# Kernel optimization log

Hardware: AMD Instinct MI355X
Metric: run time of the kernel (lower is better)

The kernel has to match this reference:

```python
import jax, jax.numpy as jnp
import numpy as np

K = 20          # args.k
NEG = 0.2       # LeakyReLU negative slope

def lrelu(x):
    return jnp.where(x >= 0, x, NEG * x)

def bn(x, s, b):
    # eval-mode batchnorm folded into per-channel affine; channel axis = 1
    sh = (1, -1) + (1,) * (x.ndim - 2)
    return x * s.reshape(sh) + b.reshape(sh)

def se(x, w1, w2):
    # Squeeze-and-Excite on (B, C, N, k)
    y = jnp.mean(x, axis=(2, 3))                      # (B, C)
    y = jax.nn.sigmoid(jax.nn.relu(y @ w1.T) @ w2.T)  # (B, C)
    return x * y[:, :, None, None]

def graph_feature(x):
    # x: (B, C, N) -> edge features (B, 2C, N, K)
    xx = jnp.sum(x * x, axis=1)                        # (B, N)
    inner = jnp.einsum('bcn,bcm->bnm', x, x)           # (B, N, N)
    dist = -xx[:, :, None] + 2.0 * inner - xx[:, None, :]
    idx = jax.lax.top_k(dist, K)[1]                    # (B, N, K) nearest (incl. self)
    xt = jnp.transpose(x, (0, 2, 1))                   # (B, N, C)
    nbr = jax.vmap(lambda t, i: t[i])(xt, idx)         # (B, N, K, C)
    ctr = xt[:, :, None, :]
    out = jnp.concatenate([nbr - ctr, jnp.broadcast_to(ctr, nbr.shape)], axis=3)
    return jnp.transpose(out, (0, 3, 1, 2))

def edge_block(x, w, s, b, w1, w2):
    # get_graph_feature -> 1x1 conv -> BN -> SE -> LeakyReLU -> max over k
    g = graph_feature(x)                               # (B, 2C, N, K)
    h = jnp.einsum('bcnk,oc->bonk', g, w)
    h = lrelu(se(bn(h, s, b), w1, w2))
    return jnp.max(h, axis=-1)                         # (B, O, N)

def forward(x, conv1_w, conv2_w, conv3_w, conv4_w, conv5_w,
            bn1_s, bn1_b, bn2_s, bn2_b, bn3_s, bn3_b, bn4_s, bn4_b, bn5_s, bn5_b,
            se1_w1, se1_w2, se2_w1, se2_w2, se3_w1, se3_w2, se4_w1, se4_w2,
            res1_w, res2_w, res3_w,
            lin1_w, bn6_s, bn6_b, lin2_w, lin2_b, bn7_s, bn7_b, lin3_w, lin3_b):
    x1 = edge_block(x, conv1_w, bn1_s, bn1_b, se1_w1, se1_w2)                 # (B,512,N)
    x2 = edge_block(x1, conv2_w, bn2_s, bn2_b, se2_w1, se2_w2)
    x2 = x2 + jnp.einsum('bcn,oc->bon', x1, res1_w)                           # (B,512,N)
    x3 = edge_block(x2, conv3_w, bn3_s, bn3_b, se3_w1, se3_w2)
    x3 = x3 + jnp.einsum('bcn,oc->bon', x2, res2_w)                           # (B,1024,N)
    x4 = edge_block(x3, conv4_w, bn4_s, bn4_b, se4_w1, se4_w2)
    x4 = x4 + jnp.einsum('bcn,oc->bon', x3, res3_w)                           # (B,1024,N)
    h = jnp.concatenate([x1, x2, x3, x4], axis=1)                             # (B,3072,N)
    h = lrelu(bn(jnp.einsum('bcn,oc->bon', h, conv5_w), bn5_s, bn5_b))        # (B,2048,N)
    f = jnp.concatenate([jnp.max(h, axis=-1), jnp.mean(h, axis=-1)], axis=1)  # (B,4096)
    f = lrelu(bn(f @ lin1_w.T, bn6_s, bn6_b))       # dropout is eval-mode identity
    f = lrelu(bn(f @ lin2_w.T + lin2_b, bn7_s, bn7_b))
    return f @ lin3_w.T + lin3_b                    # (B,40)

def setup_inputs():
    ks = jax.random.split(jax.random.key(0), 40)
    B, N = 16, 128
    f32 = jnp.float32
    def w(i, shape, s=0.02):
        return jax.random.normal(ks[i], shape, f32) * s
    def bns(i, c):
        return 1.0 + 0.1 * jax.random.normal(ks[i], (c,), f32)
    def bnb(i, c):
        return 0.1 * jax.random.normal(ks[i], (c,), f32)
    return {
        'x': jax.random.normal(ks[0], (B, 512, N), f32),
        'conv1_w': w(1, (512, 1024)),
        'conv2_w': w(2, (512, 1024)),
        'conv3_w': w(3, (1024, 1024)),
        'conv4_w': w(4, (1024, 2048)),
        'conv5_w': w(5, (2048, 3072)),
        'bn1_s': bns(6, 512), 'bn1_b': bnb(7, 512),
        'bn2_s': bns(8, 512), 'bn2_b': bnb(9, 512),
        'bn3_s': bns(10, 1024), 'bn3_b': bnb(11, 1024),
        'bn4_s': bns(12, 1024), 'bn4_b': bnb(13, 1024),
        'bn5_s': bns(14, 2048), 'bn5_b': bnb(15, 2048),
        'se1_w1': w(16, (32, 512), 0.05), 'se1_w2': w(17, (512, 32), 0.05),
        'se2_w1': w(18, (32, 512), 0.05), 'se2_w2': w(19, (512, 32), 0.05),
        'se3_w1': w(20, (64, 1024), 0.05), 'se3_w2': w(21, (1024, 64), 0.05),
        'se4_w1': w(22, (64, 1024), 0.05), 'se4_w2': w(23, (1024, 64), 0.05),
        'res1_w': w(24, (512, 512)),
        'res2_w': w(25, (1024, 512)),
        'res3_w': w(26, (1024, 1024)),
        'lin1_w': w(27, (512, 4096)),
        'bn6_s': bns(28, 512), 'bn6_b': bnb(29, 512),
        'lin2_w': w(30, (256, 512)), 'lin2_b': bnb(31, 256),
        'bn7_s': bns(32, 256), 'bn7_b': bnb(33, 256),
        'lin3_w': w(34, (40, 256)), 'lin3_b': bnb(35, 40),
    }

def reference(x, conv1_w, conv2_w, conv3_w, conv4_w, conv5_w,
              bn1_s, bn1_b, bn2_s, bn2_b, bn3_s, bn3_b, bn4_s, bn4_b, bn5_s, bn5_b,
              se1_w1, se1_w2, se2_w1, se2_w2, se3_w1, se3_w2, se4_w1, se4_w2,
              res1_w, res2_w, res3_w,
              lin1_w, bn6_s, bn6_b, lin2_w, lin2_b, bn7_s, bn7_b, lin3_w, lin3_b):
    return forward(x, conv1_w, conv2_w, conv3_w, conv4_w, conv5_w,
                   bn1_s, bn1_b, bn2_s, bn2_b, bn3_s, bn3_b, bn4_s, bn4_b, bn5_s, bn5_b,
                   se1_w1, se1_w2, se2_w1, se2_w2, se3_w1, se3_w2, se4_w1, se4_w2,
                   res1_w, res2_w, res3_w,
                   lin1_w, bn6_s, bn6_b, lin2_w, lin2_b, bn7_s, bn7_b, lin3_w, lin3_b)
```

## Files before the change

### kernel.cpp

```cpp
#include <hip/hip_runtime.h>
#include <hip/hip_bf16.h>


#define BN_ALL 2048
typedef __hip_bfloat16 bf16;
typedef __attribute__((ext_vector_type(8))) short short8;
typedef __attribute__((ext_vector_type(4))) float float4v;

__device__ __forceinline__ float b2f(bf16 v) { return __bfloat162float(v); }
__device__ __forceinline__ float lrelu(float v) { return v >= 0.f ? v : 0.2f * v; }
__device__ __forceinline__ short f2bs(float v) {
    bf16 h = __float2bfloat16(v);
    return *reinterpret_cast<short*>(&h);
}

__device__ __forceinline__ float ldin(const void* p, size_t i, int isb) {
    return isb ? __bfloat162float(((const bf16*)p)[i]) : ((const float*)p)[i];
}

__device__ __forceinline__ float ld1(const float* p) { return *p; }
__device__ __forceinline__ float ld1(const bf16* p)  { return __bfloat162float(*p); }
__device__ __forceinline__ void st1(float* p, float v) { *p = v; }
__device__ __forceinline__ void st1(bf16* p, float v)  { *p = __float2bfloat16(v); }
__device__ __forceinline__ short ldbs(const float* p) { return f2bs(*p); }
__device__ __forceinline__ short ldbs(const bf16* p)  { return *(const short*)p; }

__global__ __launch_bounds__(256) void detect_dtype(const void* __restrict__ x, int* __restrict__ flag) {
    const unsigned* u = (const unsigned*)x;
    int sane = 0;
    for (int i = threadIdx.x; i < 4096; i += 256) {
        unsigned e = (u[i] >> 23) & 0xFF;
        sane += (e >= 87 && e <= 167) ? 1 : 0;
    }
    __shared__ int sh[256];
    sh[threadIdx.x] = sane;
    __syncthreads();
    for (int off = 128; off > 0; off >>= 1) {
        if (threadIdx.x < off) sh[threadIdx.x] += sh[threadIdx.x + off];
        __syncthreads();
    }
    if (threadIdx.x == 0) *flag = (sh[0] < 2048) ? 1 : 0;
}

__global__ __launch_bounds__(256) void convert_kp(const void* __restrict__ x, bf16* __restrict__ X0,
                                                  const int* __restrict__ dflag) {
    int isb = *dflag;
    int item = blockIdx.x * 256 + threadIdx.x;
    int cg = item >> 11, bn = item & 2047;
    int b = bn >> 7, n = bn & 127;
    short8 pk;
#pragma unroll
    for (int j = 0; j < 8; ++j)
        pk[j] = f2bs(ldin(x, ((size_t)(b * 512 + cg * 8 + j)) * 128 + n, isb));
    *(short8*)((short*)X0 + ((size_t)cg * BN_ALL + bn) * 8) = pk;
}

__global__ __launch_bounds__(256) void gram_k(const bf16* __restrict__ X, int C,
                                              float* __restrict__ G) {
    __shared__ short Bsm[2][4096];
    int tid = threadIdx.x;
    int b = blockIdx.x, strip = blockIdx.y;
    int lane = tid & 63, wv = tid >> 6, wm = wv & 1, wn = wv >> 1;
    int lq = lane >> 4, lr = lane & 15;
    int KC = C >> 5;
    const short* Xs = (const short*)X;

    float4v acc[4];
#pragma unroll
    for (int i = 0; i < 4; i++) acc[i] = (float4v){0.f, 0.f, 0.f, 0.f};

    short8 br2[2];
#pragma unroll
    for (int it = 0; it < 2; ++it) {
        int i = tid + it * 256;
        int q = i >> 7, c = i & 127;
        *(short8*)&Bsm[0][(size_t)i * 8] =
            *(const short8*)(Xs + ((size_t)q * BN_ALL + b * 128 + c) * 8);
    }
    __syncthreads();

    int p = 0;
    for (int kc = 0; kc < KC; ++kc) {
        if (kc + 1 < KC) {
#pragma unroll
            for (int it = 0; it < 2; ++it) {
                int i = tid + it * 256;
                int q = i >> 7, c = i & 127;
                br2[it] = *(const short8*)(Xs + ((size_t)((kc + 1) * 4 + q) * BN_ALL + b * 128 + c) * 8);
            }
        }
        short8 av[4], bv;
#pragma unroll
        for (int mt = 0; mt < 4; ++mt)
            av[mt] = *(const short8*)&Bsm[p][(size_t)((lq << 7) + wm * 64 + mt * 16 + lr) * 8];
        bv = *(const short8*)&Bsm[p][(size_t)((lq << 7) + strip * 32 + wn * 16 + lr) * 8];
#pragma unroll
        for (int mt = 0; mt < 4; ++mt)
            acc[mt] = __builtin_amdgcn_mfma_f32_16x16x32_bf16(av[mt], bv, acc[mt], 0, 0, 0);
        if (kc + 1 < KC) {
#pragma unroll
            for (int it = 0; it < 2; ++it)
                *(short8*)&Bsm[p ^ 1][(size_t)(tid + it * 256) * 8] = br2[it];
        }
        __syncthreads();
        p ^= 1;
    }

    float* Gb = G + (size_t)b * 16384;
#pragma unroll
    for (int mt = 0; mt < 4; ++mt)
#pragma unroll
        for (int r = 0; r < 4; ++r) {
            int row = wm * 64 + mt * 16 + lq * 4 + r;
            int col = strip * 32 + wn * 16 + lr;
            Gb[row * 128 + col] = acc[mt][r];
        }
}

__global__ __launch_bounds__(256) void topk_k(const float* __restrict__ G, int* __restrict__ idx) {
    int gw = (blockIdx.x * 256 + threadIdx.x) >> 6;
    int lane = threadIdx.x & 63;
    int b = gw >> 7, n = gw & 127;
    const float* Gb = G + (size_t)b * 16384;
    float g0 = Gb[n * 128 + lane];
    float g1 = Gb[n * 128 + 64 + lane];
    float dnn = Gb[n * 129];
    float dm0 = Gb[lane * 129];
    float dm1 = Gb[(64 + lane) * 129];
    float d0 = 2.f * g0 - dnn - dm0;
    float d1 = 2.f * g1 - dnn - dm1;
#pragma unroll
    for (int k = 0; k < 20; ++k) {
        float v; int i;
        if (d1 > d0) { v = d1; i = 64 + lane; } else { v = d0; i = lane; }
#pragma unroll
        for (int off = 1; off < 64; off <<= 1) {
            float ov = __shfl_xor(v, off, 64);
            int   oi = __shfl_xor(i, off, 64);
            if (ov > v || (ov == v && oi < i)) { v = ov; i = oi; }
        }
        if (lane == 0) idx[gw * 20 + k] = i;
        if (i < 64) { if (lane == i) d0 = -3.0e38f; }
        else        { if (lane == i - 64) d1 = -3.0e38f; }
    }
}

template <typename S>
__global__ __launch_bounds__(128) void knn_topk(const S* __restrict__ X, int C, int* __restrict__ idx) {
    int b = blockIdx.x >> 7;
    int n = blockIdx.x & 127;
    int m = threadIdx.x;
    const S* base = X + b * 128;
    float s0 = 0, s1 = 0, q0 = 0, q1 = 0;
    for (int c = 0; c < C; c += 2) {
        const S* p = base + (size_t)c * BN_ALL;
        float xm0 = ld1(p + m),          xn0 = ld1(p + n);
        float xm1 = ld1(p + BN_ALL + m), xn1 = ld1(p + BN_ALL + n);
        s0 += xm0 * xn0; q0 += xm0 * xm0;
        s1 += xm1 * xn1; q1 += xm1 * xm1;
    }
    float inner = s0 + s1;
    float xxm   = q0 + q1;
    __shared__ float xx[128];
    __shared__ float dist[128];
    __shared__ float rv[128];
    __shared__ int   ri[128];
    xx[m] = xxm;
    __syncthreads();
    dist[m] = 2.0f * inner - xx[n] - xxm;
    for (int k = 0; k < 20; k++) {
        __syncthreads();
        rv[m] = dist[m]; ri[m] = m;
        __syncthreads();
        for (int off = 64; off > 0; off >>= 1) {
            if (m < off) {
                float a = rv[m], bv = rv[m + off];
                int ia = ri[m], ib = ri[m + off];
                if (bv > a || (bv == a && ib < ia)) { rv[m] = bv; ri[m] = ib; }
            }
            __syncthreads();
        }
        if (m == 0) { idx[blockIdx.x * 20 + k] = ri[0]; dist[ri[0]] = -3.0e38f; }
    }
}

__global__ __launch_bounds__(256) void pack_w(const void* __restrict__ w, int ldw,
                                              const void* __restrict__ res, int Cin, int O,
                                              int Mtot, int K, short* __restrict__ out,
                                              const int* __restrict__ dflag) {
    int isb = *dflag;
    int item = blockIdx.x * 256 + threadIdx.x;
    if (item >= Mtot * (K >> 3)) return;
    int m_local = item & 127;
    int rest = item >> 7;
    int q = rest & 3; rest >>= 2;
    int KC = K >> 5;
    int kc = rest % KC, tm = rest / KC;
    int grow = tm * 128 + m_local;
    int k = kc * 32 + q * 8;
    const void* src; size_t base; int dif = 0;
    if (grow < O)          { src = w;   base = (size_t)grow * ldw + k; }
    else if (grow < 2 * O) { src = w;   base = (size_t)(grow - O) * ldw + k; dif = 1; }
    else                   { src = res; base = (size_t)(grow - 2 * O) * Cin + k; }
    short8 pk;
#pragma unroll
    for (int j = 0; j < 8; ++j) {
        float v = ldin(src, base + j, isb);
        if (dif) v = ldin(src, base + Cin + j, isb) - v;
        pk[j] = f2bs(v);
    }
    *(short8*)&out[(size_t)item * 8] = pk;
}

__global__ __launch_bounds__(256) void gemm_p2(const short* __restrict__ packA,
                                               const bf16* __restrict__ X, float* __restrict__ Cm, int K,
                                               const void* __restrict__ bnS, const void* __restrict__ bnB,
                                               int act, const int* __restrict__ dflag) {
    __shared__ short Asm[2][4096];
    __shared__ short Bsm[2][4096];
    int tid = threadIdx.x;
    int bm  = blockIdx.x << 7;
    int bn0 = blockIdx.y << 7;
    int lane = tid & 63, wv = tid >> 6, wm = wv & 1, wn = wv >> 1;
    int lq = lane >> 4, lr = lane & 15;
    int KC = K >> 5;
    const short* abase = packA + (size_t)blockIdx.x * KC * 4096;
    const short* Xs = (const short*)X;

    float4v acc[4][4];
#pragma unroll
    for (int i = 0; i < 4; i++)
#pragma unroll
        for (int j = 0; j < 4; j++) acc[i][j] = (float4v){0.f, 0.f, 0.f, 0.f};

    short8 ar[2], br[2];
    int bq = tid >> 7, bc = tid & 127;

#pragma unroll
    for (int it = 0; it < 2; ++it) {
        ar[it] = *(const short8*)&abase[(size_t)(tid + it * 256) * 8];
        br[it] = *(const short8*)(Xs + ((size_t)(bq + it * 2) * BN_ALL + bn0 + bc) * 8);
    }
#pragma unroll
    for (int it = 0; it < 2; ++it) {
        *(short8*)&Asm[0][(size_t)(tid + it * 256) * 8] = ar[it];
        *(short8*)&Bsm[0][(size_t)(tid + it * 256) * 8] = br[it];
    }
    __syncthreads();

    int p = 0;
    for (int kc = 0; kc < KC; ++kc) {
        if (kc + 1 < KC) {
            const short* ab = abase + (size_t)(kc + 1) * 4096;
#pragma unroll
            for (int it = 0; it < 2; ++it) {
                ar[it] = *(const short8*)&ab[(size_t)(tid + it * 256) * 8];
                br[it] = *(const short8*)(Xs + ((size_t)((kc + 1) * 4 + bq + it * 2) * BN_ALL + bn0 + bc) * 8);
            }
        }
        short8 av[4], bv[4];
#pragma unroll
        for (int mt = 0; mt < 4; ++mt)
            av[mt] = *(const short8*)&Asm[p][(size_t)((lq << 7) + wm * 64 + mt * 16 + lr) * 8];
#pragma unroll
        for (int nt = 0; nt < 4; ++nt)
            bv[nt] = *(const short8*)&Bsm[p][(size_t)((lq << 7) + wn * 64 + nt * 16 + lr) * 8];
#pragma unroll
        for (int mt = 0; mt < 4; ++mt)
#pragma unroll
            for (int nt = 0; nt < 4; ++nt)
                acc[mt][nt] = __builtin_amdgcn_mfma_f32_16x16x32_bf16(av[mt], bv[nt], acc[mt][nt], 0, 0, 0);
        if (kc + 1 < KC) {
#pragma unroll
            for (int it = 0; it < 2; ++it) {
                *(short8*)&Asm[p ^ 1][(size_t)(tid + it * 256) * 8] = ar[it];
                *(short8*)&Bsm[p ^ 1][(size_t)(tid + it * 256) * 8] = br[it];
            }
        }
        __syncthreads();
        p ^= 1;
    }

    int isb = *dflag;
#pragma unroll
    for (int mt = 0; mt < 4; ++mt) {
#pragma unroll
        for (int r = 0; r < 4; ++r) {
            int row = bm + wm * 64 + mt * 16 + lq * 4 + r;
            float s = 1.f, bb = 0.f;
            if (bnS) { s = ldin(bnS, row, isb); bb = ldin(bnB, row, isb); }
#pragma unroll
            for (int nt = 0; nt < 4; ++nt) {
                int col = bn0 + wn * 64 + nt * 16 + lr;
                float v = acc[mt][nt][r];
                if (bnS) v = v * s + bb;
                if (act) v = lrelu(v);
                Cm[(size_t)row * BN_ALL + col] = v;
            }
        }
    }
}

template <typename S>
__global__ __launch_bounds__(256) void gemm_mfma(const void* __restrict__ w, int ldw,
                                                 const void* __restrict__ res, int Cin, int O,
                                                 const S* __restrict__ X, S* __restrict__ Cm, int K,
                                                 const void* __restrict__ bnS, const void* __restrict__ bnB,
                                                 int act, const int* __restrict__ dflag) {
    int isb = *dflag;
    __shared__ short Asm[4096];
    __shared__ short Bsm[4096];
    int tid = threadIdx.x;
    int bm  = blockIdx.x << 7;
    int bn0 = blockIdx.y << 7;
    int lane = tid & 63, wv = tid >> 6;
    int wm = wv & 1, wn = wv >> 1;
    int lq = lane >> 4, lr = lane & 15;

    float4v acc[4][4];
#pragma unroll
    for (int i = 0; i < 4; i++)
#pragma unroll
        for (int j = 0; j < 4; j++) acc[i][j] = (float4v){0.f, 0.f, 0.f, 0.f};

    for (int k0 = 0; k0 < K; k0 += 32) {
#pragma unroll
        for (int it = 0; it < 2; ++it) {
            int i = tid + it * 256;
            int m = i >> 2, q = i & 3;
            int grow = bm + m;
            const void* asrc; size_t abase; int dif = 0;
            if (grow < O)          { asrc = w;   abase = (size_t)grow * ldw; }
            else if (grow < 2 * O) { asrc = w;   abase = (size_t)(grow - O) * ldw; dif = 1; }
            else                   { asrc = res; abase = (size_t)(grow - 2 * O) * Cin; }
            size_t kk = (size_t)k0 + q * 8;
            short8 pk;
#pragma unroll
            for (int j = 0; j < 8; ++j) {
                float v = ldin(asrc, abase + kk + j, isb);
                if (dif) v = ldin(asrc, abase + Cin + kk + j, isb) - v;
                pk[j] = f2bs(v);
            }
            *(short8*)&Asm[(size_t)(q * 128 + m) * 8] = pk;
        }
#pragma unroll
        for (int it = 0; it < 2; ++it) {
            int i = tid + it * 256;
            int q = i >> 7, c = i & 127;
            const S* xp = X + (size_t)(k0 + q * 8) * BN_ALL + bn0 + c;
            short8 pk;
#pragma unroll
            for (int j = 0; j < 8; ++j) pk[j] = f2bs(ld1(xp + (size_t)j * BN_ALL));
            *(short8*)&Bsm[(size_t)i * 8] = pk;
        }
        __syncthreads();
        short8 av[4], bv[4];
#pragma unroll
        for (int mt = 0; mt < 4; ++mt)
            av[mt] = *(const short8*)&Asm[(size_t)((lq << 7) + wm * 64 + mt * 16 + lr) * 8];
#pragma unroll
        for (int nt = 0; nt < 4; ++nt)
            bv[nt] = *(const short8*)&Bsm[(size_t)((lq << 7) + wn * 64 + nt * 16 + lr) * 8];
#pragma unroll
        for (int mt = 0; mt < 4; ++mt)
#pragma unroll
            for (int nt = 0; nt < 4; ++nt)
                acc[mt][nt] = __builtin_amdgcn_mfma_f32_16x16x32_bf16(av[mt], bv[nt], acc[mt][nt], 0, 0, 0);
        __syncthreads();
    }
#pragma unroll
    for (int mt = 0; mt < 4; ++mt) {
#pragma unroll
        for (int r = 0; r < 4; ++r) {
            int row = bm + wm * 64 + mt * 16 + lq * 4 + r;
            float s = 1.f, bb = 0.f;
            if (bnS) { s = ldin(bnS, row, isb); bb = ldin(bnB, row, isb); }
#pragma unroll
            for (int nt = 0; nt < 4; ++nt) {
                int col = bn0 + wn * 64 + nt * 16 + lr;
                float v = acc[mt][nt][r];
                if (bnS) v = v * s + bb;
                if (act) v = lrelu(v);
                st1(Cm + (size_t)row * BN_ALL + col, v);
            }
        }
    }
}

template <typename S>
__global__ __launch_bounds__(128) void gather_pool(S* __restrict__ PS, const int* __restrict__ idx,
                                                   const void* __restrict__ bns, const void* __restrict__ bnb,
                                                   float* __restrict__ Mb, int O,
                                                   const int* __restrict__ dflag) {
    int isb = *dflag;
    int o = blockIdx.x, b = blockIdx.y, n = threadIdx.x;
    S* Prow = PS + (size_t)o * BN_ALL + b * 128;
    const int* id = idx + (b * 128 + n) * 20;
    float mx = -3.0e38f, mn = 3.0e38f, sm = 0.f;
#pragma unroll
    for (int k = 0; k < 20; k++) {
        float p = ld1(Prow + id[k]);
        mx = fmaxf(mx, p); mn = fminf(mn, p); sm += p;
    }
    float Sv = ld1(PS + (size_t)(O + o) * BN_ALL + b * 128 + n);
    __shared__ float r1[128], r2[128];
    r1[n] = sm; r2[n] = Sv;
    __syncthreads();
    float s = ldin(bns, o, isb), bb = ldin(bnb, o, isb);
    float ext = (s >= 0.f) ? mx : mn;
    st1(Prow + n, lrelu(s * (ext + Sv) + bb));
    for (int off = 64; off > 0; off >>= 1) {
        if (n < off) { r1[n] += r1[n + off]; r2[n] += r2[n + off]; }
        __syncthreads();
    }
    if (n == 0) Mb[b * O + o] = s * (r1[0] * (1.f / 2560.f) + r2[0] * (1.f / 128.f)) + bb;
}

__global__ __launch_bounds__(256) void se1_k(const float* __restrict__ Mb, const void* __restrict__ w1,
                                             float* __restrict__ Z, int O, int r,
                                             const int* __restrict__ dflag) {
    int isb = *dflag;
    int gw = (blockIdx.x * 256 + threadIdx.x) >> 6;
    int lane = threadIdx.x & 63;
    int b = gw / r, t = gw - b * r;
    const float* mv = Mb + (size_t)b * O;
    float acc = 0.f;
    for (int c = lane; c < O; c += 64) acc += ldin(w1, (size_t)t * O + c, isb) * mv[c];
#pragma unroll
    for (int off = 32; off > 0; off >>= 1) acc += __shfl_xor(acc, off, 64);
    if (lane == 0) Z[b * r + t] = fmaxf(acc, 0.f);
}

__global__ __launch_bounds__(256) void se2_k(const float* __restrict__ Z, const void* __restrict__ w2,
                                             float* __restrict__ Y, int O, int r,
                                             const int* __restrict__ dflag) {
    int isb = *dflag;
    int gw = (blockIdx.x * 256 + threadIdx.x) >> 6;
    int lane = threadIdx.x & 63;
    int b = gw / O, o = gw - b * O;
    float acc = 0.f;
    if (lane < r) acc = ldin(w2, (size_t)o * r + lane, isb) * Z[b * r + lane];
#pragma unroll
    for (int off = 32; off > 0; off >>= 1) acc += __shfl_xor(acc, off, 64);
    if (lane == 0) Y[b * O + o] = 1.f / (1.f + expf(-acc));
}

__global__ __launch_bounds__(256) void se_k(const float* __restrict__ Mb, const void* __restrict__ w1,
                                            const void* __restrict__ w2, float* __restrict__ Y, int O, int r,
                                            const int* __restrict__ dflag) {
    int isb = *dflag;
    int b = blockIdx.x, t = threadIdx.x;
    __shared__ float mloc[1024];
    __shared__ float z[64];
    for (int i = t; i < O; i += 256) mloc[i] = Mb[b * O + i];
    __syncthreads();
    if (t < r) {
        float acc = 0.f;
        for (int c = 0; c < O; c++) acc += ldin(w1, (size_t)t * O + c, isb) * mloc[c];
        z[t] = fmaxf(acc, 0.f);
    }
    __syncthreads();
    for (int o = t; o < O; o += 256) {
        float acc = 0.f;
        for (int j = 0; j < r; j++) acc += ldin(w2, (size_t)o * r + j, isb) * z[j];
        Y[b * O + o] = 1.f / (1.f + expf(-acc));
    }
}

__global__ __launch_bounds__(256) void finalize_kp(const float* __restrict__ PS, const float* __restrict__ Y,
                                                   int useR, bf16* __restrict__ Xdst, int O) {
    int item = blockIdx.x * 256 + threadIdx.x;
    int og = item >> 11, bn = item & 2047;
    int b = bn >> 7;
    short8 pk;
#pragma unroll
    for (int j = 0; j < 8; ++j) {
        int r = og * 8 + j;
        float v = Y[b * O + r] * PS[(size_t)r * BN_ALL + bn];
        if (useR) v += PS[(size_t)(2 * O + r) * BN_ALL + bn];
        pk[j] = f2bs(v);
    }
    *(short8*)((short*)Xdst + ((size_t)og * BN_ALL + bn) * 8) = pk;
}

template <typename SP, typename SD>
__global__ __launch_bounds__(256) void finalize(const SP* __restrict__ PS, const float* __restrict__ Y,
                                                int useR, SD* __restrict__ Xdst, int O) {
    int tid = blockIdx.x * 256 + threadIdx.x;
    int o = tid >> 11, bn = tid & 2047;
    int b = bn >> 7;
    float v = Y[b * O + o] * ld1(PS + tid);
    if (useR) v += ld1(PS + (size_t)(2 * O + o) * BN_ALL + bn);
    st1(Xdst + tid, v);
}

template <typename S>
__global__ __launch_bounds__(256) void convert_x(const void* __restrict__ x, S* __restrict__ X0,
                                                 const int* __restrict__ dflag) {
    int isb = *dflag;
    int tid = blockIdx.x * 256 + threadIdx.x;
    int c = tid >> 11, bn = tid & 2047;
    int b = bn >> 7, n = bn & 127;
    st1(X0 + tid, ldin(x, (size_t)(b * 512 + c) * 128 + n, isb));
}

template <typename S>
__global__ __launch_bounds__(128) void pool5(const S* __restrict__ H, float* __restrict__ f) {
    int m = blockIdx.x, b = blockIdx.y, n = threadIdx.x;
    float v = ld1(H + (size_t)m * BN_ALL + b * 128 + n);
    __shared__ float rmx[128], rsm[128];
    rmx[n] = v; rsm[n] = v;
    __syncthreads();
    for (int off = 64; off > 0; off >>= 1) {
        if (n < off) { rmx[n] = fmaxf(rmx[n], rmx[n + off]); rsm[n] += rsm[n + off]; }
        __syncthreads();
    }
    if (n == 0) {
        f[b * 4096 + m] = rmx[0];
        f[b * 4096 + 2048 + m] = rsm[0] * (1.f / 128.f);
    }
}

__global__ __launch_bounds__(256) void head_k(const float* __restrict__ in, const void* __restrict__ W,
                                              const void* __restrict__ bias, const void* __restrict__ bns,
                                              const void* __restrict__ bnb, float* __restrict__ outf,
                                              void* __restrict__ outb, int Kd, int Od, int act,
                                              const int* __restrict__ dflag) {
    int isb = *dflag;
    int gw = (blockIdx.x * 256 + threadIdx.x) >> 6;
    int lane = threadIdx.x & 63;
    if (gw >= 16 * Od) return;
    int b = gw / Od, o = gw - b * Od;
    const float* iv = in + b * Kd;
    float acc = 0.f;
    for (int k = lane; k < Kd; k += 64) acc += iv[k] * ldin(W, (size_t)o * Kd + k, isb);
    for (int off = 32; off > 0; off >>= 1) acc += __shfl_xor(acc, off, 64);
    if (lane == 0) {
        float v = acc;
        if (bias) v += ldin(bias, o, isb);
        if (bns) v = v * ldin(bns, o, isb) + ldin(bnb, o, isb);
        if (act) v = lrelu(v);
        if (outb) {
            if (isb) ((bf16*)outb)[gw] = __float2bfloat16(v);
            else     ((float*)outb)[gw] = v;
        } else outf[gw] = v;
    }
}

__global__ __launch_bounds__(256) void zero_out(bf16* o, int n) {
    int i = blockIdx.x * 256 + threadIdx.x;
    if (i < n) o[i] = __float2bfloat16(0.f);
}

#define UNPACK_INPUTS()                                                     \
    const void* x_in   = d_in[0];                                           \
    const void* conv1w = d_in[1];  const void* conv2w = d_in[2];            \
    const void* conv3w = d_in[3];  const void* conv4w = d_in[4];            \
    const void* conv5w = d_in[5];                                           \
    const void* bn1s = d_in[6],  * bn1b = d_in[7];                          \
    const void* bn2s = d_in[8],  * bn2b = d_in[9];                          \
    const void* bn3s = d_in[10], * bn3b = d_in[11];                         \
    const void* bn4s = d_in[12], * bn4b = d_in[13];                         \
    const void* bn5s = d_in[14], * bn5b = d_in[15];                         \
    const void* se1w1 = d_in[16], * se1w2 = d_in[17];                       \
    const void* se2w1 = d_in[18], * se2w2 = d_in[19];                       \
    const void* se3w1 = d_in[20], * se3w2 = d_in[21];                       \
    const void* se4w1 = d_in[22], * se4w2 = d_in[23];                       \
    const void* res1w = d_in[24]; const void* res2w = d_in[25];             \
    const void* res3w = d_in[26]; const void* lin1w = d_in[27];             \
    const void* bn6s = d_in[28], * bn6b = d_in[29];                         \
    const void* lin2w = d_in[30], * lin2b = d_in[31];                       \
    const void* bn7s = d_in[32], * bn7b = d_in[33];                         \
    const void* lin3w = d_in[34], * lin3b = d_in[35];

static void run_net_packed(void* const* d_in, void* d_out, void* d_ws, hipStream_t stream) {
    UNPACK_INPUTS();
    float* WS = (float*)d_ws;
    float* PS   = WS;
    bf16*  XC   = (bf16*)(WS + 6291456);
    short* PACK = (short*)(WS + 12582912);
    float* MB = WS + 15728640;
    float* YB = MB + 16384;
    float* FB = YB + 16384;
    float* F1 = FB + 65536;
    float* F2 = F1 + 8192;
    int* IDX  = (int*)(F2 + 4096);
    int* DFLAG = IDX + 40960;
    float* ZB = (float*)(DFLAG + 16);
    bf16*  X0 = (bf16*)(PS + (size_t)2048 * BN_ALL);
    float* GRAM = PS;
    bf16* X1 = XC;
    bf16* X2 = XC + (size_t)512 * BN_ALL;
    bf16* X3 = XC + (size_t)1024 * BN_ALL;
    bf16* X4 = XC + (size_t)2048 * BN_ALL;

    detect_dtype<<<1, 256, 0, stream>>>(x_in, DFLAG);
    convert_kp<<<512, 256, 0, stream>>>(x_in, X0, DFLAG);

    gram_k<<<dim3(16, 4), 256, 0, stream>>>(X0, 512, GRAM);
    topk_k<<<512, 256, 0, stream>>>(GRAM, IDX);
    pack_w<<<256, 256, 0, stream>>>(conv1w, 1024, nullptr, 512, 512, 1024, 512, PACK, DFLAG);
    gemm_p2<<<dim3(8, 16), 256, 0, stream>>>(PACK, X0, PS, 512, nullptr, nullptr, 0, DFLAG);
    gather_pool<float><<<dim3(512, 16), 128, 0, stream>>>(PS, IDX, bn1s, bn1b, MB, 512, DFLAG);
    se1_k<<<128, 256, 0, stream>>>(MB, se1w1, ZB, 512, 32, DFLAG);
    se2_k<<<2048, 256, 0, stream>>>(ZB, se1w2, YB, 512, 32, DFLAG);
    finalize_kp<<<512, 256, 0, stream>>>(PS, YB, 0, X1, 512);

    gram_k<<<dim3(16, 4), 256, 0, stream>>>(X1, 512, GRAM);
    topk_k<<<512, 256, 0, stream>>>(GRAM, IDX);
    pack_w<<<384, 256, 0, stream>>>(conv2w, 1024, res1w, 512, 512, 1536, 512, PACK, DFLAG);
    gemm_p2<<<dim3(12, 16), 256, 0, stream>>>(PACK, X1, PS, 512, nullptr, nullptr, 0, DFLAG);
    gather_pool<float><<<dim3(512, 16), 128, 0, stream>>>(PS, IDX, bn2s, bn2b, MB, 512, DFLAG);
    se1_k<<<128, 256, 0, stream>>>(MB, se2w1, ZB, 512, 32, DFLAG);
    se2_k<<<2048, 256, 0, stream>>>(ZB, se2w2, YB, 512, 32, DFLAG);
    finalize_kp<<<512, 256, 0, stream>>>(PS, YB, 1, X2, 512);

    gram_k<<<dim3(16, 4), 256, 0, stream>>>(X2, 512, GRAM);
    topk_k<<<512, 256, 0, stream>>>(GRAM, IDX);
    pack_w<<<768, 256, 0, stream>>>(conv3w, 1024, res2w, 512, 1024, 3072, 512, PACK, DFLAG);
    gemm_p2<<<dim3(24, 16), 256, 0, stream>>>(PACK, X2, PS, 512, nullptr, nullptr, 0, DFLAG);
    gather_pool<float><<<dim3(1024, 16), 128, 0, stream>>>(PS, IDX, bn3s, bn3b, MB, 1024, DFLAG);
    se1_k<<<256, 256, 0, stream>>>(MB, se3w1, ZB, 1024, 64, DFLAG);
    se2_k<<<4096, 256, 0, stream>>>(ZB, se3w2, YB, 1024, 64, DFLAG);
    finalize_kp<<<1024, 256, 0, stream>>>(PS, YB, 1, X3, 1024);

    gram_k<<<dim3(16, 4), 256, 0, stream>>>(X3, 1024, GRAM);
    topk_k<<<512, 256, 0, stream>>>(GRAM, IDX);
    pack_w<<<1536, 256, 0, stream>>>(conv4w, 2048, res3w, 1024, 1024, 3072, 1024, PACK, DFLAG);
    gemm_p2<<<dim3(24, 16), 256, 0, stream>>>(PACK, X3, PS, 1024, nullptr, nullptr, 0, DFLAG);
    gather_pool<float><<<dim3(1024, 16), 128, 0, stream>>>(PS, IDX, bn4s, bn4b, MB, 1024, DFLAG);
    se1_k<<<256, 256, 0, stream>>>(MB, se4w1, ZB, 1024, 64, DFLAG);
    se2_k<<<4096, 256, 0, stream>>>(ZB, se4w2, YB, 1024, 64, DFLAG);
    finalize_kp<<<1024, 256, 0, stream>>>(PS, YB, 1, X4, 1024);

    pack_w<<<3072, 256, 0, stream>>>(conv5w, 3072, nullptr, 3072, 2048, 2048, 3072, PACK, DFLAG);
    gemm_p2<<<dim3(16, 16), 256, 0, stream>>>(PACK, XC, PS, 3072, bn5s, bn5b, 1, DFLAG);
    pool5<float><<<dim3(2048, 16), 128, 0, stream>>>(PS, FB);

    head_k<<<2048, 256, 0, stream>>>(FB, lin1w, nullptr, bn6s, bn6b, F1, nullptr, 4096, 512, 1, DFLAG);
    head_k<<<1024, 256, 0, stream>>>(F1, lin2w, lin2b, bn7s, bn7b, F2, nullptr, 512, 256, 1, DFLAG);
    head_k<<<160, 256, 0, stream>>>(F2, lin3w, lin3b, nullptr, nullptr, nullptr, d_out, 256, 40, 0, DFLAG);
}

template <typename S>
static void run_net(void* const* d_in, void* d_out, void* d_ws, hipStream_t stream) {
    UNPACK_INPUTS();
    const size_t RC = (size_t)3072 * BN_ALL;
    S* PS = (S*)d_ws;
    S* XC = PS + RC;
    S* X0 = PS + (size_t)2048 * BN_ALL;
    float* MB = (float*)(XC + RC);
    float* YB = MB + 16 * 1024;
    float* FB = YB + 16 * 1024;
    float* F1 = FB + 16 * 4096;
    float* F2 = F1 + 16 * 512;
    int* IDX  = (int*)(F2 + 16 * 256);
    int* DFLAG = IDX + 16 * 128 * 20;

    S* X1 = XC;
    S* X2 = XC + (size_t)512 * BN_ALL;
    S* X3 = XC + (size_t)1024 * BN_ALL;
    S* X4 = XC + (size_t)2048 * BN_ALL;

    detect_dtype<<<1, 256, 0, stream>>>(x_in, DFLAG);
    convert_x<S><<<4096, 256, 0, stream>>>(x_in, X0, DFLAG);

    knn_topk<S><<<2048, 128, 0, stream>>>(X0, 512, IDX);
    gemm_mfma<S><<<dim3(8, 16), 256, 0, stream>>>(conv1w, 1024, nullptr, 512, 512, X0, PS, 512, nullptr, nullptr, 0, DFLAG);
    gather_pool<S><<<dim3(512, 16), 128, 0, stream>>>(PS, IDX, bn1s, bn1b, MB, 512, DFLAG);
    se_k<<<16, 256, 0, stream>>>(MB, se1w1, se1w2, YB, 512, 32, DFLAG);
    finalize<S, S><<<4096, 256, 0, stream>>>(PS, YB, 0, X1, 512);

    knn_topk<S><<<2048, 128, 0, stream>>>(X1, 512, IDX);
    gemm_mfma<S><<<dim3(12, 16), 256, 0, stream>>>(conv2w, 1024, res1w, 512, 512, X1, PS, 512, nullptr, nullptr, 0, DFLAG);
    gather_pool<S><<<dim3(512, 16), 128, 0, stream>>>(PS, IDX, bn2s, bn2b, MB, 512, DFLAG);
    se_k<<<16, 256, 0, stream>>>(MB, se2w1, se2w2, YB, 512, 32, DFLAG);
    finalize<S, S><<<4096, 256, 0, stream>>>(PS, YB, 1, X2, 512);

    knn_topk<S><<<2048, 128, 0, stream>>>(X2, 512, IDX);
    gemm_mfma<S><<<dim3(24, 16), 256, 0, stream>>>(conv3w, 1024, res2w, 512, 1024, X2, PS, 512, nullptr, nullptr, 0, DFLAG);
    gather_pool<S><<<dim3(1024, 16), 128, 0, stream>>>(PS, IDX, bn3s, bn3b, MB, 1024, DFLAG);
    se_k<<<16, 256, 0, stream>>>(MB, se3w1, se3w2, YB, 1024, 64, DFLAG);
    finalize<S, S><<<8192, 256, 0, stream>>>(PS, YB, 1, X3, 1024);

    knn_topk<S><<<2048, 128, 0, stream>>>(X3, 1024, IDX);
    gemm_mfma<S><<<dim3(24, 16), 256, 0, stream>>>(conv4w, 2048, res3w, 1024, 1024, X3, PS, 1024, nullptr, nullptr, 0, DFLAG);
    gather_pool<S><<<dim3(1024, 16), 128, 0, stream>>>(PS, IDX, bn4s, bn4b, MB, 1024, DFLAG);
    se_k<<<16, 256, 0, stream>>>(MB, se4w1, se4w2, YB, 1024, 64, DFLAG);
    finalize<S, S><<<8192, 256, 0, stream>>>(PS, YB, 1, X4, 1024);

    gemm_mfma<S><<<dim3(16, 16), 256, 0, stream>>>(conv5w, 3072, nullptr, 3072, 2048, XC, PS, 3072, bn5s, bn5b, 1, DFLAG);
    pool5<S><<<dim3(2048, 16), 128, 0, stream>>>(PS, FB);

    head_k<<<2048, 256, 0, stream>>>(FB, lin1w, nullptr, bn6s, bn6b, F1, nullptr, 4096, 512, 1, DFLAG);
    head_k<<<1024, 256, 0, stream>>>(F1, lin2w, lin2b, bn7s, bn7b, F2, nullptr, 512, 256, 1, DFLAG);
    head_k<<<160, 256, 0, stream>>>(F2, lin3w, lin3b, nullptr, nullptr, nullptr, d_out, 256, 40, 0, DFLAG);
}

extern "C" void kernel_launch(void* const* d_in, const int* in_sizes, int n_in,
                              void* d_out, int out_size, void* d_ws, size_t ws_size,
                              hipStream_t stream) {
    const size_t SMALL = (16 * 1024 + 16 * 1024 + 16 * 4096 + 16 * 512 + 16 * 256) * 4
                       + 16 * 128 * 20 * 4 + 8192;
    const size_t NEED_PACKED = (size_t)15728640 * 4 + SMALL;
    const size_t NEED_F32    = 2 * ((size_t)3072 * BN_ALL * 4) + SMALL;
    const size_t NEED_BF16   = 2 * ((size_t)3072 * BN_ALL * 2) + SMALL;
    if (ws_size >= NEED_PACKED) {
        run_net_packed(d_in, d_out, d_ws, stream);
    } else if (ws_size >= NEED_F32) {
        run_net<float>(d_in, d_out, d_ws, stream);
    } else if (ws_size >= NEED_BF16) {
        run_net<bf16>(d_in, d_out, d_ws, stream);
    } else {
        zero_out<<<3, 256, 0, stream>>>((bf16*)d_out, out_size);
    }
}
```

Measured before the change: 646.5 us.

## Replace LDS-staged GEMM with register-direct 4-stage pipelined MFMA and async gram loads

The main GEMM drops shared-memory staging. Each wave now loads its MFMA fragments directly from global memory into registers, using a 4-deep software pipeline, and the N tile is halved to 64 so the grid has twice as many blocks. The gram kernel uses global_load_lds async copies, when the builtin is available, in place of register round-trips into LDS. This removes LDS writes and barriers in the GEMM, at the cost of redundant global loads across waves (no LDS sharing) and higher register pressure from the buffered fragments.

```diff
diff --git a/kernel.cpp b/kernel.cpp
--- a/kernel.cpp
+++ b/kernel.cpp
@@ -6,6 +6,20 @@
 typedef __hip_bfloat16 bf16;
 typedef __attribute__((ext_vector_type(8))) short short8;
 typedef __attribute__((ext_vector_type(4))) float float4v;
+
+#if defined(__has_builtin)
+#if __has_builtin(__builtin_amdgcn_global_load_lds)
+#define HAS_GLL 1
+#endif
+#endif
+
+#ifdef HAS_GLL
+__device__ __forceinline__ void gll16(const void* g, void* l) {
+    __builtin_amdgcn_global_load_lds(
+        (const __attribute__((address_space(1))) void*)g,
+        (__attribute__((address_space(3))) void*)l, 16, 0, 0);
+}
+#endif
 
 __device__ __forceinline__ float b2f(bf16 v) { return __bfloat162float(v); }
 __device__ __forceinline__ float lrelu(float v) { return v >= 0.f ? v : 0.2f * v; }
@@ -22,8 +36,6 @@
 __device__ __forceinline__ float ld1(const bf16* p)  { return __bfloat162float(*p); }
 __device__ __forceinline__ void st1(float* p, float v) { *p = v; }
 __device__ __forceinline__ void st1(bf16* p, float v)  { *p = __float2bfloat16(v); }
-__device__ __forceinline__ short ldbs(const float* p) { return f2bs(*p); }
-__device__ __forceinline__ short ldbs(const bf16* p)  { return *(const short*)p; }
 
 __global__ __launch_bounds__(256) void detect_dtype(const void* __restrict__ x, int* __restrict__ flag) {
     const unsigned* u = (const unsigned*)x;
@@ -57,7 +69,7 @@
 
 __global__ __launch_bounds__(256) void gram_k(const bf16* __restrict__ X, int C,
                                               float* __restrict__ G) {
-    __shared__ short Bsm[2][4096];
+    __shared__ __align__(16) short Bsm[2][4096];
     int tid = threadIdx.x;
     int b = blockIdx.x, strip = blockIdx.y;
     int lane = tid & 63, wv = tid >> 6, wm = wv & 1, wn = wv >> 1;
@@ -69,6 +81,37 @@
 #pragma unroll
     for (int i = 0; i < 4; i++) acc[i] = (float4v){0.f, 0.f, 0.f, 0.f};
 
+#ifdef HAS_GLL
+#pragma unroll
+    for (int it = 0; it < 2; ++it) {
+        int i = tid + it * 256;
+        int q = i >> 7, c = i & 127;
+        gll16(Xs + ((size_t)q * BN_ALL + b * 128 + c) * 8, &Bsm[0][(size_t)i * 8]);
+    }
+    __syncthreads();
+    int p = 0;
+    for (int kc = 0; kc < KC; ++kc) {
+        if (kc + 1 < KC) {
+#pragma unroll
+            for (int it = 0; it < 2; ++it) {
+                int i = tid + it * 256;
+                int q = i >> 7, c = i & 127;
+                gll16(Xs + ((size_t)((kc + 1) * 4 + q) * BN_ALL + b * 128 + c) * 8,
+                      &Bsm[p ^ 1][(size_t)i * 8]);
+            }
+        }
+        short8 av[4], bv;
+#pragma unroll
+        for (int mt = 0; mt < 4; ++mt)
+            av[mt] = *(const short8*)&Bsm[p][(size_t)((lq << 7) + wm * 64 + mt * 16 + lr) * 8];
+        bv = *(const short8*)&Bsm[p][(size_t)((lq << 7) + strip * 32 + wn * 16 + lr) * 8];
+#pragma unroll
+        for (int mt = 0; mt < 4; ++mt)
+            acc[mt] = __builtin_amdgcn_mfma_f32_16x16x32_bf16(av[mt], bv, acc[mt], 0, 0, 0);
+        __syncthreads();
+        p ^= 1;
+    }
+#else
     short8 br2[2];
 #pragma unroll
     for (int it = 0; it < 2; ++it) {
@@ -78,7 +121,6 @@
             *(const short8*)(Xs + ((size_t)q * BN_ALL + b * 128 + c) * 8);
     }
     __syncthreads();
-
     int p = 0;
     for (int kc = 0; kc < KC; ++kc) {
         if (kc + 1 < KC) {
@@ -105,6 +147,7 @@
         __syncthreads();
         p ^= 1;
     }
+#endif
 
     float* Gb = G + (size_t)b * 16384;
 #pragma unroll
@@ -212,73 +255,57 @@
     *(short8*)&out[(size_t)item * 8] = pk;
 }
 
-__global__ __launch_bounds__(256) void gemm_p2(const short* __restrict__ packA,
+#define LOADK(kc_, s_) do {                                                        \
+    int _kc = (kc_);                                                               \
+    if (_kc < KC) {                                                                \
+        const short* _ab = abase + (size_t)_kc * 4096;                             \
+        _Pragma("unroll")                                                          \
+        for (int mt = 0; mt < 4; ++mt) bufA[s_][mt] = *(const short8*)(_ab + aoff[mt]); \
+        const short* _bb = Xs + (size_t)(_kc * 4 + lq) * (BN_ALL * 8);             \
+        _Pragma("unroll")                                                          \
+        for (int nt = 0; nt < 2; ++nt) bufB[s_][nt] = *(const short8*)(_bb + boff[nt]); \
+    } } while (0)
+#define MFMAK(s_) do {                                                             \
+    _Pragma("unroll")                                                              \
+    for (int mt = 0; mt < 4; ++mt)                                                 \
+        _Pragma("unroll")                                                          \
+        for (int nt = 0; nt < 2; ++nt)                                             \
+            acc[mt][nt] = __builtin_amdgcn_mfma_f32_16x16x32_bf16(bufA[s_][mt], bufB[s_][nt], acc[mt][nt], 0, 0, 0); \
+    } while (0)
+
+__global__ __launch_bounds__(256) void gemm_dr(const short* __restrict__ packA,
                                                const bf16* __restrict__ X, float* __restrict__ Cm, int K,
                                                const void* __restrict__ bnS, const void* __restrict__ bnB,
                                                int act, const int* __restrict__ dflag) {
-    __shared__ short Asm[2][4096];
-    __shared__ short Bsm[2][4096];
     int tid = threadIdx.x;
     int bm  = blockIdx.x << 7;
-    int bn0 = blockIdx.y << 7;
+    int bn0 = blockIdx.y << 6;
     int lane = tid & 63, wv = tid >> 6, wm = wv & 1, wn = wv >> 1;
     int lq = lane >> 4, lr = lane & 15;
     int KC = K >> 5;
     const short* abase = packA + (size_t)blockIdx.x * KC * 4096;
     const short* Xs = (const short*)X;
 
-    float4v acc[4][4];
+    int aoff[4], boff[2];
+#pragma unroll
+    for (int mt = 0; mt < 4; ++mt) aoff[mt] = ((lq << 7) + wm * 64 + mt * 16 + lr) * 8;
+#pragma unroll
+    for (int nt = 0; nt < 2; ++nt) boff[nt] = (bn0 + wn * 32 + nt * 16 + lr) * 8;
+
+    float4v acc[4][2];
 #pragma unroll
     for (int i = 0; i < 4; i++)
 #pragma unroll
-        for (int j = 0; j < 4; j++) acc[i][j] = (float4v){0.f, 0.f, 0.f, 0.f};
-
-    short8 ar[2], br[2];
-    int bq = tid >> 7, bc = tid & 127;
-
-#pragma unroll
-    for (int it = 0; it < 2; ++it) {
-        ar[it] = *(const short8*)&abase[(size_t)(tid + it * 256) * 8];
-        br[it] = *(const short8*)(Xs + ((size_t)(bq + it * 2) * BN_ALL + bn0 + bc) * 8);
-    }
-#pragma unroll
-    for (int it = 0; it < 2; ++it) {
-        *(short8*)&Asm[0][(size_t)(tid + it * 256) * 8] = ar[it];
-        *(short8*)&Bsm[0][(size_t)(tid + it * 256) * 8] = br[it];
-    }
-    __syncthreads();
-
-    int p = 0;
-    for (int kc = 0; kc < KC; ++kc) {
-        if (kc + 1 < KC) {
-            const short* ab = abase + (size_t)(kc + 1) * 4096;
-#pragma unroll
-            for (int it = 0; it < 2; ++it) {
-                ar[it] = *(const short8*)&ab[(size_t)(tid + it * 256) * 8];
-                br[it] = *(const short8*)(Xs + ((size_t)((kc + 1) * 4 + bq + it * 2) * BN_ALL + bn0 + bc) * 8);
-            }
-        }
-        short8 av[4], bv[4];
-#pragma unroll
-        for (int mt = 0; mt < 4; ++mt)
-            av[mt] = *(const short8*)&Asm[p][(size_t)((lq << 7) + wm * 64 + mt * 16 + lr) * 8];
-#pragma unroll
-        for (int nt = 0; nt < 4; ++nt)
-            bv[nt] = *(const short8*)&Bsm[p][(size_t)((lq << 7) + wn * 64 + nt * 16 + lr) * 8];
-#pragma unroll
-        for (int mt = 0; mt < 4; ++mt)
-#pragma unroll
-            for (int nt = 0; nt < 4; ++nt)
-                acc[mt][nt] = __builtin_amdgcn_mfma_f32_16x16x32_bf16(av[mt], bv[nt], acc[mt][nt], 0, 0, 0);
-        if (kc + 1 < KC) {
-#pragma unroll
-            for (int it = 0; it < 2; ++it) {
-                *(short8*)&Asm[p ^ 1][(size_t)(tid + it * 256) * 8] = ar[it];
-                *(short8*)&Bsm[p ^ 1][(size_t)(tid + it * 256) * 8] = br[it];
-            }
-        }
-        __syncthreads();
-        p ^= 1;
+        for (int j = 0; j < 2; j++) acc[i][j] = (float4v){0.f, 0.f, 0.f, 0.f};
+
+    short8 bufA[4][4], bufB[4][2];
+    LOADK(0, 0);
+    LOADK(1, 1);
+    for (int kc0 = 0; kc0 < KC; kc0 += 4) {
+        LOADK(kc0 + 2, 2); MFMAK(0);
+        LOADK(kc0 + 3, 3); MFMAK(1);
+        LOADK(kc0 + 4, 0); MFMAK(2);
+        LOADK(kc0 + 5, 1); MFMAK(3);
     }
 
     int isb = *dflag;
@@ -290,8 +317,8 @@
             float s = 1.f, bb = 0.f;
             if (bnS) { s = ldin(bnS, row, isb); bb = ldin(bnB, row, isb); }
 #pragma unroll
-            for (int nt = 0; nt < 4; ++nt) {
-                int col = bn0 + wn * 64 + nt * 16 + lr;
+            for (int nt = 0; nt < 2; ++nt) {
+                int col = bn0 + wn * 32 + nt * 16 + lr;
                 float v = acc[mt][nt][r];
                 if (bnS) v = v * s + bb;
                 if (act) v = lrelu(v);
@@ -600,7 +627,7 @@
     gram_k<<<dim3(16, 4), 256, 0, stream>>>(X0, 512, GRAM);
     topk_k<<<512, 256, 0, stream>>>(GRAM, IDX);
     pack_w<<<256, 256, 0, stream>>>(conv1w, 1024, nullptr, 512, 512, 1024, 512, PACK, DFLAG);
-    gemm_p2<<<dim3(8, 16), 256, 0, stream>>>(PACK, X0, PS, 512, nullptr, nullptr, 0, DFLAG);
+    gemm_dr<<<dim3(8, 32), 256, 0, stream>>>(PACK, X0, PS, 512, nullptr, nullptr, 0, DFLAG);
     gather_pool<float><<<dim3(512, 16), 128, 0, stream>>>(PS, IDX, bn1s, bn1b, MB, 512, DFLAG);
     se1_k<<<128, 256, 0, stream>>>(MB, se1w1, ZB, 512, 32, DFLAG);
     se2_k<<<2048, 256, 0, stream>>>(ZB, se1w2, YB, 512, 32, DFLAG);
@@ -609,7 +636,7 @@
     gram_k<<<dim3(16, 4), 256, 0, stream>>>(X1, 512, GRAM);
     topk_k<<<512, 256, 0, stream>>>(GRAM, IDX);
     pack_w<<<384, 256, 0, stream>>>(conv2w, 1024, res1w, 512, 512, 1536, 512, PACK, DFLAG);
-    gemm_p2<<<dim3(12, 16), 256, 0, stream>>>(PACK, X1, PS, 512, nullptr, nullptr, 0, DFLAG);
+    gemm_dr<<<dim3(12, 32), 256, 0, stream>>>(PACK, X1, PS, 512, nullptr, nullptr, 0, DFLAG);
     gather_pool<float><<<dim3(512, 16), 128, 0, stream>>>(PS, IDX, bn2s, bn2b, MB, 512, DFLAG);
     se1_k<<<128, 256, 0, stream>>>(MB, se2w1, ZB, 512, 32, DFLAG);
     se2_k<<<2048, 256, 0, stream>>>(ZB, se2w2, YB, 512, 32, DFLAG);
@@ -618,7 +645,7 @@
     gram_k<<<dim3(16, 4), 256, 0, stream>>>(X2, 512, GRAM);
     topk_k<<<512, 256, 0, stream>>>(GRAM, IDX);
     pack_w<<<768, 256, 0, stream>>>(conv3w, 1024, res2w, 512, 1024, 3072, 512, PACK, DFLAG);
-    gemm_p2<<<dim3(24, 16), 256, 0, stream>>>(PACK, X2, PS, 512, nullptr, nullptr, 0, DFLAG);
+    gemm_dr<<<dim3(24, 32), 256, 0, stream>>>(PACK, X2, PS, 512, nullptr, nullptr, 0, DFLAG);
     gather_pool<float><<<dim3(1024, 16), 128, 0, stream>>>(PS, IDX, bn3s, bn3b, MB, 1024, DFLAG);
     se1_k<<<256, 256, 0, stream>>>(MB, se3w1, ZB, 1024, 64, DFLAG);
     se2_k<<<4096, 256, 0, stream>>>(ZB, se3w2, YB, 1024, 64, DFLAG);
@@ -627,14 +654,14 @@
     gram_k<<<dim3(16, 4), 256, 0, stream>>>(X3, 1024, GRAM);
     topk_k<<<512, 256, 0, stream>>>(GRAM, IDX);
     pack_w<<<1536, 256, 0, stream>>>(conv4w, 2048, res3w, 1024, 1024, 3072, 1024, PACK, DFLAG);
-    gemm_p2<<<dim3(24, 16), 256, 0, stream>>>(PACK, X3, PS, 1024, nullptr, nullptr, 0, DFLAG);
+    gemm_dr<<<dim3(24, 32), 256, 0, stream>>>(PACK, X3, PS, 1024, nullptr, nullptr, 0, DFLAG);
     gather_pool<float><<<dim3(1024, 16), 128, 0, stream>>>(PS, IDX, bn4s, bn4b, MB, 1024, DFLAG);
     se1_k<<<256, 256, 0, stream>>>(MB, se4w1, ZB, 1024, 64, DFLAG);
     se2_k<<<4096, 256, 0, stream>>>(ZB, se4w2, YB, 1024, 64, DFLAG);
     finalize_kp<<<1024, 256, 0, stream>>>(PS, YB, 1, X4, 1024);
 
     pack_w<<<3072, 256, 0, stream>>>(conv5w, 3072, nullptr, 3072, 2048, 2048, 3072, PACK, DFLAG);
-    gemm_p2<<<dim3(16, 16), 256, 0, stream>>>(PACK, XC, PS, 3072, bn5s, bn5b, 1, DFLAG);
+    gemm_dr<<<dim3(16, 32), 256, 0, stream>>>(PACK, XC, PS, 3072, bn5s, bn5b, 1, DFLAG);
     pool5<float><<<dim3(2048, 16), 128, 0, stream>>>(PS, FB);
 
     head_k<<<2048, 256, 0, stream>>>(FB, lin1w, nullptr, bn6s, bn6b, F1, nullptr, 4096, 512, 1, DFLAG);
```

New measurement: 627.4 us. 2.9% less time.
